# Optimization experiments

Measured on AMD Instinct MI355X. Metric: run time of the kernel, lower is better.

## Reference

```python
import jax, jax.numpy as jnp
import numpy as np

B, T, I, H, O = 256, 256, 16, 256, 11
HYP_HID = 512
BLD = 8
N1 = H * I + H * H + 2 * H        # RNN cell params (W_ih, W_hh, b_ih, b_hh)
N2 = O * H + O                    # readout params (W_out, b_out)


def setup_inputs() -> dict:
    key = jax.random.key(0)
    k = jax.random.split(key, 4)
    bld = jax.random.normal(k[0], (B, BLD), dtype=jnp.float32)
    stimulus = jax.random.normal(k[1], (B, T, I), dtype=jnp.float32)
    # hypnet MLP: bld -> relu -> flat per-sample params; small init to keep tanh unsaturated
    W1 = jax.random.normal(k[2], (BLD, HYP_HID), dtype=jnp.float32) * 0.05
    b1 = jnp.zeros((HYP_HID,), dtype=jnp.float32)
    W2 = jax.random.normal(k[3], (HYP_HID, N1 + N2), dtype=jnp.float32) * 0.02
    b2 = jnp.zeros((N1 + N2,), dtype=jnp.float32)
    return {"bld": bld, "stimulus": stimulus, "W1": W1, "b1": b1, "W2": W2, "b2": b2}


def reference(bld, stimulus, W1, b1, W2, b2):
    # hypernetwork: per-sample flat params [B, N1+N2]
    flat = jax.nn.relu(bld @ W1 + b1) @ W2 + b2
    params1, params2 = flat[:, :N1], flat[:, N1:]

    # unpack per-sample RNN cell params
    o = 0
    W_ih = params1[:, o:o + H * I].reshape(B, H, I); o += H * I
    W_hh = params1[:, o:o + H * H].reshape(B, H, H); o += H * H
    b_ih = params1[:, o:o + H]; o += H
    b_hh = params1[:, o:o + H]
    W_out = params2[:, :O * H].reshape(B, O, H)
    b_out = params2[:, O * H:].reshape(B, O)

    # shift stimulus right by one step with a zero frame (teacher forcing input)
    rnn_input = jnp.concatenate(
        [jnp.zeros((B, 1, I), dtype=stimulus.dtype), stimulus[:, :-1]], axis=1)

    # precompute input projection for all steps: [B, T, H]
    x_proj = jnp.einsum('bti,bhi->bth', rnn_input, W_ih) + b_ih[:, None, :]

    def step(h, xp_t):  # h: [B, H], xp_t: [B, H]
        h_next = jnp.tanh(xp_t + jnp.einsum('bh,bgh->bg', h, W_hh) + b_hh)
        return h_next, h_next

    h0 = jnp.zeros((B, H), dtype=stimulus.dtype)
    h_last, out_tm = jax.lax.scan(step, h0, jnp.swapaxes(x_proj, 0, 1))
    output1 = jnp.swapaxes(out_tm, 0, 1)  # [B, T, H]

    # per-sample linear readout [B, T, O]
    output2 = jnp.einsum('bth,boh->bto', output1, W_out) + b_out[:, None, :]
    output2 = jnp.nan_to_num(output2, nan=0.0)

    output_act = jax.nn.sigmoid(output2[:, :, :3])
    output_bldi = output2[:, :, 3:]
    h = h_last[None]  # [1, B, H]
    return (output_act, output_bldi, h, params1, params2)
```

## Files before the change

### kernel.cpp

```cpp
#include <hip/hip_runtime.h>

typedef unsigned short u16;
typedef unsigned int u32;
using short8   = __attribute__((ext_vector_type(8))) short;
using floatx4  = __attribute__((ext_vector_type(4))) float;
using half_t   = _Float16;
using half2_t  = __attribute__((ext_vector_type(2))) _Float16;
using halfx8   = __attribute__((ext_vector_type(8))) _Float16;

constexpr int B_ = 256, T_ = 256, I_ = 16, H_ = 256, O_ = 11;
constexpr int HYP = 512;
constexpr int N1_ = H_ * I_ + H_ * H_ + 2 * H_;
constexpr int N2_ = O_ * H_ + O_;
constexpr int GN  = N1_ + N2_;

constexpr size_t OUT_ACT  = 0;
constexpr size_t OUT_BLDI = (size_t)B_ * T_ * 3;
constexpr size_t OUT_H    = OUT_BLDI + (size_t)B_ * T_ * 8;
constexpr size_t OUT_P1   = OUT_H + (size_t)B_ * H_;
constexpr size_t OUT_P2   = OUT_P1 + (size_t)B_ * N1_;

__device__ inline void bar_lds() {
    asm volatile("s_waitcnt lgkmcnt(0)\n\ts_barrier" ::: "memory");
}

__device__ inline float bf2f(u16 u) {
    union { u32 i; float f; } v; v.i = ((u32)u) << 16; return v.f;
}
__device__ inline u16 f2bf(float f) {
    u32 x = __float_as_uint(f);
    u32 r = (x + 0x7fffu + ((x >> 16) & 1u)) >> 16;
    return (u16)r;
}

__device__ inline bool sniff_f32(const void* p) {
    const u16* w = (const u16*)p;
    const int lane = threadIdx.x & 63;
    u16 u = w[lane * 2];
    unsigned e = (u >> 7) & 0xFF;
    bool inband = (u == 0) || (e >= 77 && e <= 140);
    return __popcll(__ballot(inband)) < 56;
}

__device__ inline float ldr(const void* p, size_t i, bool f32) {
    return f32 ? ((const float*)p)[i] : bf2f(((const u16*)p)[i]);
}

__global__ void h1_kernel(const void* __restrict__ bld, const void* __restrict__ W1,
                          const void* __restrict__ b1, u16* __restrict__ h1) {
    const bool bldf = sniff_f32(bld);
    const bool w1f  = sniff_f32(W1);
    const bool b1f  = sniff_f32(b1);
    const int b = blockIdx.x;
    const int j = threadIdx.x;
    float acc = ldr(b1, j, b1f);
#pragma unroll
    for (int k = 0; k < 8; k++)
        acc += ldr(bld, b * 8 + k, bldf) * ldr(W1, k * HYP + j, w1f);
    h1[b * HYP + j] = f2bf(fmaxf(acc, 0.f));
}

constexpr int KS_ = 32;
constexpr int NST = HYP / KS_;
constexpr int TKP = 40;

template<bool W2F32>
__device__ void gemm_body(const u16* __restrict__ A, const void* __restrict__ Bm,
                          const void* __restrict__ b2, bool b2f,
                          float* __restrict__ out) {
    __shared__ alignas(16) u16 tileT[2][64][TKP];

    const int nb   = blockIdx.x * 64;
    const int tid  = threadIdx.x;
    const int lane = tid & 63;
    const int wid  = tid >> 6;
    const int l15  = lane & 15;
    const int q    = lane >> 4;

    int  col[4]; bool cv[4];
#pragma unroll
    for (int j = 0; j < 4; j++) {
        int c = nb + j * 16 + l15;
        cv[j]  = (c < GN);
        col[j] = cv[j] ? c : (GN - 1);
    }

    const u16* ap[4];
#pragma unroll
    for (int i = 0; i < 4; i++)
        ap[i] = A + (wid * 64 + i * 16 + l15) * HYP + q * 8;

    const int scol_i = tid & 63;
    const int kq     = tid >> 6;
    int gc = nb + scol_i;
    if (gc >= GN) gc = GN - 1;
    const size_t colOff = (size_t)gc;

    float pfw[8]; u16 pbw[8];
    short8 afc[4];

    {
        float t0[8]; u16 t1[8];
#pragma unroll
        for (int e = 0; e < 8; e++) {
            const size_t ro = (size_t)(kq * 8 + e) * (size_t)GN + colOff;
            if constexpr (W2F32) t0[e] = ((const float*)Bm)[ro];
            else                 t1[e] = ((const u16*)Bm)[ro];
        }
        short8 wv8;
#pragma unroll
        for (int e = 0; e < 8; e++) {
            if constexpr (W2F32) wv8[e] = (short)f2bf(t0[e]);
            else                 wv8[e] = (short)t1[e];
        }
        *(short8*)&tileT[0][scol_i][kq * 8] = wv8;
    }
#pragma unroll
    for (int e = 0; e < 8; e++) {
        const size_t ro = (size_t)(KS_ + kq * 8 + e) * (size_t)GN + colOff;
        if constexpr (W2F32) pfw[e] = ((const float*)Bm)[ro];
        else                 pbw[e] = ((const u16*)Bm)[ro];
    }
#pragma unroll
    for (int i = 0; i < 4; i++) afc[i] = *(const short8*)(ap[i]);
    bar_lds();

    floatx4 acc[4][4] = {};

#pragma unroll
    for (int ks = 0; ks < NST; ks++) {
        const int cur = ks & 1;

        short8 bfr[4];
#pragma unroll
        for (int j = 0; j < 4; j++)
            bfr[j] = *(const short8*)&tileT[cur][j * 16 + l15][q * 8];

        short8 afn[4];
        if (ks + 1 < NST) {
#pragma unroll
            for (int i = 0; i < 4; i++)
                afn[i] = *(const short8*)(ap[i] + (ks + 1) * KS_);
        }
        float pfn[8]; u16 pbn[8];
        if (ks + 2 < NST) {
#pragma unroll
            for (int e = 0; e < 8; e++) {
                const size_t ro = (size_t)((ks + 2) * KS_ + kq * 8 + e) * (size_t)GN + colOff;
                if constexpr (W2F32) pfn[e] = ((const float*)Bm)[ro];
                else                 pbn[e] = ((const u16*)Bm)[ro];
            }
        }
        if (ks + 1 < NST) {
            short8 wv8;
#pragma unroll
            for (int e = 0; e < 8; e++) {
                if constexpr (W2F32) wv8[e] = (short)f2bf(pfw[e]);
                else                 wv8[e] = (short)pbw[e];
            }
            *(short8*)&tileT[cur ^ 1][scol_i][kq * 8] = wv8;
        }

#pragma unroll
        for (int i = 0; i < 4; i++)
#pragma unroll
            for (int j = 0; j < 4; j++)
                acc[i][j] = __builtin_amdgcn_mfma_f32_16x16x32_bf16(afc[i], bfr[j], acc[i][j], 0, 0, 0);
        bar_lds();

#pragma unroll
        for (int i = 0; i < 4; i++) afc[i] = afn[i];
#pragma unroll
        for (int e = 0; e < 8; e++) {
            if constexpr (W2F32) pfw[e] = pfn[e];
            else                 pbw[e] = pbn[e];
        }
    }

    const bool isP2 = (nb >= N1_);
#pragma unroll
    for (int j = 0; j < 4; j++) {
        const float bias = ldr(b2, col[j], b2f);
#pragma unroll
        for (int i = 0; i < 4; i++) {
            const int mbase = wid * 64 + i * 16 + q * 4;
#pragma unroll
            for (int r = 0; r < 4; r++) {
                if (cv[j]) {
                    const float v = acc[i][j][r] + bias;
                    const int m = mbase + r;
                    size_t dst;
                    if (isP2) dst = OUT_P2 + (size_t)m * N2_ + (size_t)(col[j] - N1_);
                    else      dst = OUT_P1 + (size_t)m * N1_ + (size_t)col[j];
                    out[dst] = v;
                }
            }
        }
    }
}
__global__ __launch_bounds__(256) void gemm_kernel(const u16* A, const void* Bm,
                                                   const void* b2, float* out) {
    const bool w2f = sniff_f32(Bm);
    const bool b2f = sniff_f32(b2);
    if (w2f) gemm_body<true>(A, Bm, b2, b2f, out);
    else     gemm_body<false>(A, Bm, b2, b2f, out);
}

constexpr int HROW = 256;
constexpr int XROW = 40;

__global__ __launch_bounds__(512, 1) void rnn_kernel(const void* __restrict__ stim,
                                                     float* __restrict__ out) {
    const bool stf = sniff_f32(stim);
    const int b    = blockIdx.x;
    const int tid  = threadIdx.x;
    const int lane = tid & 63;
    const int wv   = tid >> 6;
    const int l15  = lane & 15;
    const int q    = lane >> 4;

    const float* p1 = out + OUT_P1 + (size_t)b * N1_;
    const float* p2 = out + OUT_P2 + (size_t)b * N2_;

    __shared__ alignas(16) half_t hist[(T_ + 1) * HROW];
    __shared__ alignas(16) half_t stim_s[T_ * XROW];

    if (stf) {
        const float2* sp = (const float2*)stim + (size_t)b * T_ * 8;
        for (int idx = tid; idx < (T_ - 1) * 8; idx += 512) {
            const int tt = idx >> 3, pr = idx & 7;
            float2 v = sp[idx];
            half2_t h; h.x = (half_t)v.x; h.y = (half_t)v.y;
            *(half2_t*)&stim_s[(tt + 1) * XROW + pr * 2] = h;
        }
    } else {
        const u32* sp = (const u32*)((const u16*)stim + (size_t)b * T_ * I_);
        for (int idx = tid; idx < (T_ - 1) * 8; idx += 512) {
            const int tt = idx >> 3, pr = idx & 7;
            u32 u = sp[idx];
            union { u32 i; float f; } lo2, hi2;
            lo2.i = u << 16; hi2.i = u & 0xffff0000u;
            half2_t h; h.x = (half_t)lo2.f; h.y = (half_t)hi2.f;
            *(half2_t*)&stim_s[(tt + 1) * XROW + pr * 2] = h;
        }
    }
    {
        u32* ss = (u32*)stim_s;
        if (tid < 256) {
            const int base = tid * (XROW / 2);
            ss[base + 8] = 0x00003C00u;
#pragma unroll
            for (int z = 9; z < XROW / 2; z++) ss[base + z] = 0u;
        }
        if (tid < 8)   ss[tid] = 0u;
        if (tid < 128) ((u32*)hist)[tid] = 0u;
    }

    halfx8 Wf[2][8];
    halfx8 Wx[2];
    {
        const float* WH  = p1 + H_ * I_;
        const float* BIH = p1 + H_ * I_ + H_ * H_;
#pragma unroll
        for (int it = 0; it < 2; it++) {
            const int rr = 32 * wv + it * 16 + l15;
#pragma unroll
            for (int kt = 0; kt < 8; kt++) {
                const float4* wp = (const float4*)(WH + (size_t)rr * H_ + kt * 32 + q * 8);
                float4 r0 = wp[0], r1 = wp[1];
                halfx8 f;
                f[0] = (half_t)r0.x; f[1] = (half_t)r0.y; f[2] = (half_t)r0.z; f[3] = (half_t)r0.w;
                f[4] = (half_t)r1.x; f[5] = (half_t)r1.y; f[6] = (half_t)r1.z; f[7] = (half_t)r1.w;
                Wf[it][kt] = f;
            }
            halfx8 fx;
#pragma unroll
            for (int j = 0; j < 8; j++) fx[j] = (half_t)0.f;
            if (q < 2) {
                const float4* ip = (const float4*)(p1 + (size_t)rr * I_ + q * 8);
                float4 r0 = ip[0], r1 = ip[1];
                fx[0] = (half_t)r0.x; fx[1] = (half_t)r0.y; fx[2] = (half_t)r0.z; fx[3] = (half_t)r0.w;
                fx[4] = (half_t)r1.x; fx[5] = (half_t)r1.y; fx[6] = (half_t)r1.z; fx[7] = (half_t)r1.w;
            } else if (q == 2) {
                fx[0] = (half_t)(BIH[rr] + BIH[H_ + rr]);
            }
            Wx[it] = fx;
        }
    }
    __syncthreads();

#pragma unroll
    for (int tm = 0; tm < 16; tm++) {
        halfx8 ax = *(const halfx8*)(stim_s + (size_t)(16 * tm + l15) * XROW + q * 8);
        floatx4 xa0 = __builtin_amdgcn_mfma_f32_16x16x32_f16(ax, Wx[0], floatx4{}, 0, 0, 0);
        floatx4 xa1 = __builtin_amdgcn_mfma_f32_16x16x32_f16(ax, Wx[1], floatx4{}, 0, 0, 0);
#pragma unroll
        for (int r = 0; r < 4; r++) {
            const int trow = 16 * tm + 4 * q + r;
            hist[(size_t)(trow + 1) * HROW + 32 * wv + l15]      = (half_t)xa0[r];
            hist[(size_t)(trow + 1) * HROW + 32 * wv + 16 + l15] = (half_t)xa1[r];
        }
    }
    __syncthreads();

    const int g32 = 32 * wv + (lane & 31);
    for (int t = 0; t < T_; t++) {
        halfx8 af[8];
        const half_t* hr = hist + (size_t)t * HROW + q * 8;
#pragma unroll
        for (int kt = 0; kt < 8; kt++)
            af[kt] = *(const halfx8*)(hr + kt * 32);
        const float xp = (float)hist[(size_t)(t + 1) * HROW + g32];

        floatx4 acc0 = {}, acc1 = {};
        __builtin_amdgcn_s_setprio(1);
#pragma unroll
        for (int kt = 0; kt < 8; kt++) {
            acc0 = __builtin_amdgcn_mfma_f32_16x16x32_f16(af[kt], Wf[0][kt], acc0, 0, 0, 0);
            acc1 = __builtin_amdgcn_mfma_f32_16x16x32_f16(af[kt], Wf[1][kt], acc1, 0, 0, 0);
        }
        __builtin_amdgcn_s_setprio(0);

        if (lane < 32) {
            const float s  = ((lane < 16) ? acc0[0] : acc1[0]) + xp;
            const float e  = __expf(2.f * s);
            const float hn = 1.f - 2.f / (e + 1.f);
            hist[(size_t)(t + 1) * HROW + g32] = (half_t)hn;
            if (t == T_ - 1) out[OUT_H + (size_t)b * H_ + g32] = hn;
        }
        bar_lds();
    }

    halfx8 Wo[8];
    float bo = 0.f;
    {
#pragma unroll
        for (int kt = 0; kt < 8; kt++) {
            halfx8 f;
#pragma unroll
            for (int j = 0; j < 8; j++) f[j] = (half_t)0.f;
            if (l15 < O_) {
                const float* wp = p2 + (size_t)l15 * H_ + kt * 32 + q * 8;
#pragma unroll
                for (int j = 0; j < 8; j++) f[j] = (half_t)wp[j];
            }
            Wo[kt] = f;
        }
        if (l15 < O_) bo = p2[O_ * H_ + l15];
    }

#pragma unroll
    for (int m = 0; m < 2; m++) {
        const int tb = (2 * wv + m) * 16;
        const half_t* hr = hist + (size_t)(tb + l15 + 1) * HROW + q * 8;
        floatx4 acc = {};
#pragma unroll
        for (int kt = 0; kt < 8; kt++) {
            halfx8 a = *(const halfx8*)(hr + kt * 32);
            acc = __builtin_amdgcn_mfma_f32_16x16x32_f16(a, Wo[kt], acc, 0, 0, 0);
        }
        if (l15 < O_) {
            const int o = l15;
#pragma unroll
            for (int r = 0; r < 4; r++) {
                const int tt = tb + q * 4 + r;
                float v2 = acc[r] + bo;
                if (o < 3) out[OUT_ACT + (size_t)b * T_ * 3 + (size_t)tt * 3 + o] = 1.f / (1.f + __expf(-v2));
                else       out[OUT_BLDI + (size_t)b * T_ * 8 + (size_t)tt * 8 + (o - 3)] = v2;
            }
        }
    }
}

extern "C" void kernel_launch(void* const* d_in, const int* in_sizes, int n_in,
                              void* d_out, int out_size, void* d_ws, size_t ws_size,
                              hipStream_t stream) {
    (void)in_sizes; (void)n_in; (void)out_size; (void)d_ws; (void)ws_size;
    const void* bld  = d_in[0];
    const void* stim = d_in[1];
    const void* W1   = d_in[2];
    const void* b1   = d_in[3];
    const void* W2   = d_in[4];
    const void* b2   = d_in[5];
    float* out = (float*)d_out;
    u16* h1 = (u16*)out;

    h1_kernel<<<B_, HYP, 0, stream>>>(bld, W1, b1, h1);
    gemm_kernel<<<(GN + 63) / 64, 256, 0, stream>>>(h1, W2, b2, out);
    rnn_kernel<<<B_, 512, 0, stream>>>(stim, out);
}
```

Before: 417.7 us.

## Make hypernet GEMM persistent over column chunks with deeper W2 prefetch

The hypernetwork GEMM now launches a fixed grid of 256 blocks, and each block loops over 64-column chunks of W2 instead of launching one block per chunk. The W2 register prefetch is also deepened from two to four K-steps ahead, so more global loads are in flight while the MFMAs run. The aim is to cut block launch overhead and hide memory latency on this bandwidth-bound weight stream. In exchange, each thread holds more registers, which can lower occupancy, and the chunks may be unevenly spread across blocks.

```diff
diff --git a/kernel.cpp b/kernel.cpp
--- a/kernel.cpp
+++ b/kernel.cpp
@@ -63,6 +63,7 @@
 constexpr int KS_ = 32;
 constexpr int NST = HYP / KS_;
 constexpr int TKP = 40;
+constexpr int NCH = (GN + 63) / 64;
 
 template<bool W2F32>
 __device__ void gemm_body(const u16* __restrict__ A, const void* __restrict__ Bm,
@@ -70,21 +71,12 @@
                           float* __restrict__ out) {
     __shared__ alignas(16) u16 tileT[2][64][TKP];
 
-    const int nb   = blockIdx.x * 64;
     const int tid  = threadIdx.x;
     const int lane = tid & 63;
     const int wid  = tid >> 6;
     const int l15  = lane & 15;
     const int q    = lane >> 4;
 
-    int  col[4]; bool cv[4];
-#pragma unroll
-    for (int j = 0; j < 4; j++) {
-        int c = nb + j * 16 + l15;
-        cv[j]  = (c < GN);
-        col[j] = cv[j] ? c : (GN - 1);
-    }
-
     const u16* ap[4];
 #pragma unroll
     for (int i = 0; i < 4; i++)
@@ -92,107 +84,116 @@
 
     const int scol_i = tid & 63;
     const int kq     = tid >> 6;
-    int gc = nb + scol_i;
-    if (gc >= GN) gc = GN - 1;
-    const size_t colOff = (size_t)gc;
-
-    float pfw[8]; u16 pbw[8];
-    short8 afc[4];
-
-    {
-        float t0[8]; u16 t1[8];
-#pragma unroll
-        for (int e = 0; e < 8; e++) {
-            const size_t ro = (size_t)(kq * 8 + e) * (size_t)GN + colOff;
-            if constexpr (W2F32) t0[e] = ((const float*)Bm)[ro];
-            else                 t1[e] = ((const u16*)Bm)[ro];
-        }
-        short8 wv8;
-#pragma unroll
-        for (int e = 0; e < 8; e++) {
-            if constexpr (W2F32) wv8[e] = (short)f2bf(t0[e]);
-            else                 wv8[e] = (short)t1[e];
-        }
-        *(short8*)&tileT[0][scol_i][kq * 8] = wv8;
-    }
-#pragma unroll
-    for (int e = 0; e < 8; e++) {
-        const size_t ro = (size_t)(KS_ + kq * 8 + e) * (size_t)GN + colOff;
-        if constexpr (W2F32) pfw[e] = ((const float*)Bm)[ro];
-        else                 pbw[e] = ((const u16*)Bm)[ro];
-    }
-#pragma unroll
-    for (int i = 0; i < 4; i++) afc[i] = *(const short8*)(ap[i]);
-    bar_lds();
-
-    floatx4 acc[4][4] = {};
-
-#pragma unroll
-    for (int ks = 0; ks < NST; ks++) {
-        const int cur = ks & 1;
-
-        short8 bfr[4];
-#pragma unroll
-        for (int j = 0; j < 4; j++)
-            bfr[j] = *(const short8*)&tileT[cur][j * 16 + l15][q * 8];
-
-        short8 afn[4];
-        if (ks + 1 < NST) {
+
+    for (int c = blockIdx.x; c < NCH; c += 256) {
+        const int nb = c * 64;
+
+        int  col[4]; bool cv[4];
+#pragma unroll
+        for (int j = 0; j < 4; j++) {
+            int cc = nb + j * 16 + l15;
+            cv[j]  = (cc < GN);
+            col[j] = cv[j] ? cc : (GN - 1);
+        }
+        int gc = nb + scol_i;
+        if (gc >= GN) gc = GN - 1;
+        const size_t colOff = (size_t)gc;
+
+        float pf[4][8]; u16 pb[4][8];
+        short8 afc[4];
+
+        {
+            float t0[8]; u16 t1[8];
+#pragma unroll
+            for (int e = 0; e < 8; e++) {
+                const size_t ro = (size_t)(kq * 8 + e) * (size_t)GN + colOff;
+                if constexpr (W2F32) t0[e] = ((const float*)Bm)[ro];
+                else                 t1[e] = ((const u16*)Bm)[ro];
+            }
+            short8 wv8;
+#pragma unroll
+            for (int e = 0; e < 8; e++) {
+                if constexpr (W2F32) wv8[e] = (short)f2bf(t0[e]);
+                else                 wv8[e] = (short)t1[e];
+            }
+            *(short8*)&tileT[0][scol_i][kq * 8] = wv8;
+        }
+#pragma unroll
+        for (int s = 1; s < 4; s++) {
+#pragma unroll
+            for (int e = 0; e < 8; e++) {
+                const size_t ro = (size_t)(s * KS_ + kq * 8 + e) * (size_t)GN + colOff;
+                if constexpr (W2F32) pf[s][e] = ((const float*)Bm)[ro];
+                else                 pb[s][e] = ((const u16*)Bm)[ro];
+            }
+        }
+#pragma unroll
+        for (int i = 0; i < 4; i++) afc[i] = *(const short8*)(ap[i]);
+        bar_lds();
+
+        floatx4 acc[4][4] = {};
+
+#pragma unroll
+        for (int ks = 0; ks < NST; ks++) {
+            const int cur = ks & 1;
+
+            short8 bfr[4];
+#pragma unroll
+            for (int j = 0; j < 4; j++)
+                bfr[j] = *(const short8*)&tileT[cur][j * 16 + l15][q * 8];
+
+            short8 afn[4];
+            if (ks + 1 < NST) {
+#pragma unroll
+                for (int i = 0; i < 4; i++)
+                    afn[i] = *(const short8*)(ap[i] + (ks + 1) * KS_);
+            }
+            if (ks + 4 < NST) {
+#pragma unroll
+                for (int e = 0; e < 8; e++) {
+                    const size_t ro = (size_t)((ks + 4) * KS_ + kq * 8 + e) * (size_t)GN + colOff;
+                    if constexpr (W2F32) pf[ks % 4][e] = ((const float*)Bm)[ro];
+                    else                 pb[ks % 4][e] = ((const u16*)Bm)[ro];
+                }
+            }
+            if (ks + 1 < NST) {
+                short8 wv8;
+#pragma unroll
+                for (int e = 0; e < 8; e++) {
+                    if constexpr (W2F32) wv8[e] = (short)f2bf(pf[(ks + 1) % 4][e]);
+                    else                 wv8[e] = (short)pb[(ks + 1) % 4][e];
+                }
+                *(short8*)&tileT[cur ^ 1][scol_i][kq * 8] = wv8;
+            }
+
 #pragma unroll
             for (int i = 0; i < 4; i++)
-                afn[i] = *(const short8*)(ap[i] + (ks + 1) * KS_);
-        }
-        float pfn[8]; u16 pbn[8];
-        if (ks + 2 < NST) {
-#pragma unroll
-            for (int e = 0; e < 8; e++) {
-                const size_t ro = (size_t)((ks + 2) * KS_ + kq * 8 + e) * (size_t)GN + colOff;
-                if constexpr (W2F32) pfn[e] = ((const float*)Bm)[ro];
-                else                 pbn[e] = ((const u16*)Bm)[ro];
-            }
-        }
-        if (ks + 1 < NST) {
-            short8 wv8;
-#pragma unroll
-            for (int e = 0; e < 8; e++) {
-                if constexpr (W2F32) wv8[e] = (short)f2bf(pfw[e]);
-                else                 wv8[e] = (short)pbw[e];
-            }
-            *(short8*)&tileT[cur ^ 1][scol_i][kq * 8] = wv8;
-        }
-
-#pragma unroll
-        for (int i = 0; i < 4; i++)
-#pragma unroll
-            for (int j = 0; j < 4; j++)
-                acc[i][j] = __builtin_amdgcn_mfma_f32_16x16x32_bf16(afc[i], bfr[j], acc[i][j], 0, 0, 0);
-        bar_lds();
-
-#pragma unroll
-        for (int i = 0; i < 4; i++) afc[i] = afn[i];
-#pragma unroll
-        for (int e = 0; e < 8; e++) {
-            if constexpr (W2F32) pfw[e] = pfn[e];
-            else                 pbw[e] = pbn[e];
-        }
-    }
-
-    const bool isP2 = (nb >= N1_);
-#pragma unroll
-    for (int j = 0; j < 4; j++) {
-        const float bias = ldr(b2, col[j], b2f);
-#pragma unroll
-        for (int i = 0; i < 4; i++) {
-            const int mbase = wid * 64 + i * 16 + q * 4;
-#pragma unroll
-            for (int r = 0; r < 4; r++) {
-                if (cv[j]) {
-                    const float v = acc[i][j][r] + bias;
-                    const int m = mbase + r;
-                    size_t dst;
-                    if (isP2) dst = OUT_P2 + (size_t)m * N2_ + (size_t)(col[j] - N1_);
-                    else      dst = OUT_P1 + (size_t)m * N1_ + (size_t)col[j];
-                    out[dst] = v;
+#pragma unroll
+                for (int j = 0; j < 4; j++)
+                    acc[i][j] = __builtin_amdgcn_mfma_f32_16x16x32_bf16(afc[i], bfr[j], acc[i][j], 0, 0, 0);
+            bar_lds();
+
+#pragma unroll
+            for (int i = 0; i < 4; i++) afc[i] = afn[i];
+        }
+
+        const bool isP2 = (nb >= N1_);
+#pragma unroll
+        for (int j = 0; j < 4; j++) {
+            const float bias = ldr(b2, col[j], b2f);
+#pragma unroll
+            for (int i = 0; i < 4; i++) {
+                const int mbase = wid * 64 + i * 16 + q * 4;
+#pragma unroll
+                for (int r = 0; r < 4; r++) {
+                    if (cv[j]) {
+                        const float v = acc[i][j][r] + bias;
+                        const int m = mbase + r;
+                        size_t dst;
+                        if (isP2) dst = OUT_P2 + (size_t)m * N2_ + (size_t)(col[j] - N1_);
+                        else      dst = OUT_P1 + (size_t)m * N1_ + (size_t)col[j];
+                        out[dst] = v;
+                    }
                 }
             }
         }
@@ -386,6 +387,6 @@
     u16* h1 = (u16*)out;
 
     h1_kernel<<<B_, HYP, 0, stream>>>(bld, W1, b1, h1);
-    gemm_kernel<<<(GN + 63) / 64, 256, 0, stream>>>(h1, W2, b2, out);
+    gemm_kernel<<<256, 256, 0, stream>>>(h1, W2, b2, out);
     rnn_kernel<<<B_, 512, 0, stream>>>(stim, out);
 }
```

Result: no change. 414.2 us (-0.8%).
